# Kernel tuning notes

Measured on AMD Instinct MI355X. Metric: run time of the kernel, lower is better.

The kernel has to match this reference:

```python
import jax, jax.numpy as jnp
import numpy as np

B, L, P = 16, 128, 8192
ALPHA = 2.0            # current_alpha (softness_start)
STEP_PROGRESS = 0.5    # > 0.15 so e_ghost == 0; t_gate = sigmoid(3.0)
PROT_RADII = np.array([1.7, 1.55, 1.52, 1.8], dtype=np.float32)
PROT_EPS = np.array([0.1, 0.1, 0.15, 0.2], dtype=np.float32)
VDW_RADII = np.array([1.7, 1.55, 1.52, 1.8, 1.1, 1.47, 1.75, 1.85, 1.98], dtype=np.float32)
EPSILON = np.array([0.086, 0.17, 0.21, 0.25, 0.015, 0.061, 0.265, 0.32, 0.4], dtype=np.float32)


def setup_inputs() -> dict:
    key = jax.random.key(0)
    ks = jax.random.split(key, 6)
    # positions spread over ~ a binding-pocket-sized box so distances are realistic
    pos_L = jax.random.normal(ks[0], (B, L, 3), jnp.float32) * 8.0
    pos_P = jax.random.normal(ks[1], (B, P, 3), jnp.float32) * 8.0
    q_L = jax.random.normal(ks[2], (B, L), jnp.float32) * 0.3
    q_P = jax.random.normal(ks[3], (B, P), jnp.float32) * 0.3
    x_L = jax.random.uniform(ks[4], (B, L, 9), jnp.float32)
    x_L = x_L / jnp.sum(x_L, axis=-1, keepdims=True)  # type probabilities
    x_P = jax.random.uniform(ks[5], (B, P, 4), jnp.float32)
    x_P = x_P / jnp.sum(x_P, axis=-1, keepdims=True)
    return {
        'pos_L': pos_L, 'pos_P': pos_P, 'q_L': q_L, 'q_P': q_P,
        'x_L': x_L, 'x_P': x_P,
        'vdw_radii': jnp.asarray(VDW_RADII), 'epsilon_tbl': jnp.asarray(EPSILON),
    }


def reference(pos_L, pos_P, q_L, q_P, x_L, x_P, vdw_radii, epsilon_tbl):
    sg = jax.lax.stop_gradient
    # pairwise geometry: diff [B,L,P,3]
    diff = pos_L[:, :, None, :] - pos_P[:, None, :, :]
    dist_sq = jnp.sum(diff * diff, axis=-1)              # [B,L,P]
    dist = jnp.sqrt(dist_sq + 1e-8)
    # mixed vdw radii
    type_probs_L = x_L[..., :9]
    radii_L = type_probs_L @ vdw_radii                    # [B,L]
    radii_P = x_P[..., :4] @ jnp.asarray(PROT_RADII)      # [B,P]
    sigma_ij = radii_L[:, :, None] + radii_P[:, None, :]  # [B,L,P]
    # soft-core distance
    soft_dist = jnp.sqrt(dist_sq + ALPHA * sigma_ij * sigma_ij + 1e-8)
    # electrostatics (dielectric = 4.0), tanh-clamped
    e_elec_raw = 332.06 * q_L[:, :, None] * q_P[:, None, :] / (4.0 * soft_dist)
    e_elec = 200.0 * jnp.tanh(e_elec_raw / 200.0)
    # LJ 12-6 with geometric-mean epsilon
    eps_L = jax.nn.relu(type_probs_L @ epsilon_tbl)       # [B,L]
    eps_P = x_P[..., :4] @ jnp.asarray(PROT_EPS)          # [B,P]
    eps_ij = jnp.sqrt(eps_L[:, :, None] * eps_P[:, None, :] + 1e-8)
    ratio = jnp.minimum(sigma_ij / (soft_dist + 1e-8), 5.0)
    ratio6 = ratio ** 6
    ratio12 = ratio6 * ratio6
    e_vdw_raw = 4.0 * eps_ij * (ratio12 - ratio6)
    e_pos = 500.0 * jnp.tanh(jax.nn.relu(e_vdw_raw) / 500.0)
    e_neg = -10.0 * jnp.tanh(jax.nn.relu(-e_vdw_raw) / 10.0)
    e_vdw_grad = e_pos + e_neg
    # smooth 12 A cutoff
    dist_mask = jax.nn.sigmoid((12.0 - dist) * 2.0)
    e_soft = jnp.sum((e_elec + e_vdw_grad) * dist_mask, axis=(1, 2))  # [B]
    # hydrophobic surface attraction (carbon-carbon)
    mask_cc = type_probs_L[..., 0][:, :, None] * x_P[..., 0][:, None, :]
    hsa_term = 1.0 / (1.0 + (dist / 4.0) ** 4)
    e_hsa = jnp.sum(-0.5 * mask_cc * hsa_term * dist_mask, axis=(1, 2))
    # Pauli repulsion, gated by step progress
    t_gate = jax.nn.sigmoid(jnp.float32((STEP_PROGRESS - 0.2) * 10.0))
    overlap = jax.nn.relu(sigma_ij * 0.6 - dist)
    e_pauli = t_gate * 100.0 * jnp.sum(overlap * overlap, axis=(1, 2))
    # e_ghost = 0 since STEP_PROGRESS >= 0.15
    e_ghost = jnp.zeros_like(e_pauli)
    e_raw = e_soft + 5.0 * e_hsa + e_pauli + e_ghost
    e_raw = jnp.nan_to_num(e_raw, nan=0.0)
    # logging quantities (detached in the original)
    log_vdw = jnp.clip(sg(e_vdw_raw), -10.0, 500.0)
    log_soft_core = jnp.sum((sg(e_elec) + log_vdw) * sg(dist_mask), axis=(1, 2))
    e_soft_log = jnp.clip(log_soft_core + 5.0 * sg(e_hsa), -500.0, 5000.0)
    e_hard_log = jnp.minimum(sg(e_pauli + e_ghost), 10000.0)
    log_energy_val = jnp.minimum(e_soft_log + e_hard_log, 1000000.0)
    return e_raw, e_hard_log, jnp.float32(ALPHA), log_energy_val
```

## Files before the change

kernel.cpp:

```cpp
#include <hip/hip_runtime.h>
#include <math.h>

#define NB 16
#define NL 128
#define NP 8192
#define CHUNKS 32
#define THREADS 256
#define LSPLIT 2
#define LHALF (NL / LSPLIT)

__device__ __forceinline__ float fexp2(float x) { return __builtin_amdgcn_exp2f(x); }
__device__ __forceinline__ float frcp(float x)  { return __builtin_amdgcn_rcpf(x); }
__device__ __forceinline__ float frsq(float x)  { return __builtin_amdgcn_rsqf(x); }
__device__ __forceinline__ float fsqrt_(float x){ return __builtin_amdgcn_sqrtf(x); }

__global__ __launch_bounds__(THREADS) void physics_main(
    const float* __restrict__ pos_L, const float* __restrict__ pos_P,
    const float* __restrict__ q_L,   const float* __restrict__ q_P,
    const float* __restrict__ x_L,   const float* __restrict__ x_P,
    const float* __restrict__ vdw_radii, const float* __restrict__ eps_tbl,
    float* __restrict__ partial)
{
    const int b     = blockIdx.y;
    const int chunk = blockIdx.x;
    const int z     = blockIdx.z;
    const int tid   = threadIdx.x;

    __shared__ float4 lig[LHALF][2];
    __shared__ float red[4][3];

    if (tid < LHALF) {
        const int base = b * NL + z * LHALF + tid;
        float px = pos_L[base * 3 + 0];
        float py = pos_L[base * 3 + 1];
        float pz = pos_L[base * 3 + 2];
        float aq = 83.015f * q_L[base];
        float rad = 0.0f, ep = 0.0f;
        #pragma unroll
        for (int j = 0; j < 9; ++j) {
            float v = x_L[base * 9 + j];
            rad = fmaf(v, vdw_radii[j], rad);
            ep  = fmaf(v, eps_tbl[j],  ep);
        }
        float seL4 = 4.0f * fsqrt_(fmaxf(ep, 0.0f));
        float x0   = x_L[base * 9 + 0];
        lig[tid][0] = make_float4(px, py, pz, aq);
        lig[tid][1] = make_float4(rad, seL4, x0, 0.0f);
    }
    __syncthreads();

    const int p  = chunk * THREADS + tid;
    const int pb = b * NP + p;
    const float ppx = pos_P[pb * 3 + 0];
    const float ppy = pos_P[pb * 3 + 1];
    const float ppz = pos_P[pb * 3 + 2];
    const float qP  = q_P[pb];
    const float4 xp = ((const float4*)x_P)[pb];
    const float rP  = 1.7f * xp.x + 1.55f * xp.y + 1.52f * xp.z + 1.8f * xp.w;
    const float epP = 0.1f * xp.x + 0.10f * xp.y + 0.15f * xp.z + 0.2f * xp.w;
    const float seP = fsqrt_(epP);
    const float xP0 = xp.x;

    float s1 = 0.0f, s2 = 0.0f, s3 = 0.0f;

    #pragma unroll 4
    for (int l = 0; l < LHALF; ++l) {
        const float4 a  = lig[l][0];
        const float4 bv = lig[l][1];

        float dx = a.x - ppx, dy = a.y - ppy, dz = a.z - ppz;
        float ds = fmaf(dx, dx, fmaf(dy, dy, fmaf(dz, dz, 1e-8f)));
        float dist = fsqrt_(ds);

        float sigma = bv.x + rP;
        float sd2 = fmaf(sigma, sigma + sigma, ds);
        float inv_sd = frsq(sd2);

        float v  = (a.w * qP) * inv_sd;
        float u  = 0.005f * v;
        float u2 = u * u;
        float pf = fmaf(u2, fmaf(u2, 0.13333333f, -0.33333333f), 1.0f);
        float e_elec = v * pf;

        float ratio = sigma * inv_sd;
        float r2 = ratio * ratio;
        float r6 = r2 * r2 * r2;
        float ev = (bv.y * seP) * r6 * (r6 - 1.0f);
        float addend = e_elec + ev;

        float m  = fminf(fmaf(dist, 2.8853901f, -34.624681f), 30.0f);
        float A  = 1.0f + fexp2(m);
        float tq = ds * 0.0625f;
        float Bh = fmaf(tq, tq, 1.0f);
        float r  = frcp(A * Bh);
        float dm = Bh * r;

        s1 = fmaf(addend, dm, s1);
        s2 = fmaf(bv.z, r, s2);

        float ov = fmaxf(fmaf(sigma, 0.6f, -dist), 0.0f);
        s3 = fmaf(ov, ov, s3);
    }
    s2 *= xP0;

    #pragma unroll
    for (int off = 32; off > 0; off >>= 1) {
        s1 += __shfl_down(s1, off);
        s2 += __shfl_down(s2, off);
        s3 += __shfl_down(s3, off);
    }
    const int lane = tid & 63;
    const int wid  = tid >> 6;
    if (lane == 0) {
        red[wid][0] = s1; red[wid][1] = s2; red[wid][2] = s3;
    }
    __syncthreads();
    if (tid == 0) {
        float r0 = red[0][0] + red[1][0] + red[2][0] + red[3][0];
        float r1 = red[0][1] + red[1][1] + red[2][1] + red[3][1];
        float r2_ = red[0][2] + red[1][2] + red[2][2] + red[3][2];
        float* dst = partial + ((size_t)((b * CHUNKS + chunk) * LSPLIT + z)) * 4;
        dst[0] = r0; dst[1] = r1; dst[2] = r2_;
    }
}

__global__ void physics_final(const float* __restrict__ partial, float* __restrict__ out)
{
    const int b = threadIdx.x;
    if (b == 0) out[2 * NB] = 2.0f;
    if (b >= NB) return;
    float s1 = 0.0f, s2 = 0.0f, s3 = 0.0f;
    for (int c = 0; c < CHUNKS * LSPLIT; ++c) {
        const float* src = partial + ((size_t)(b * CHUNKS * LSPLIT + c)) * 4;
        s1 += src[0]; s2 += src[1]; s3 += src[2];
    }
    const float TG100 = 95.25741268224334f;
    float e_pauli = TG100 * s3;
    float e_hsa5  = -2.5f * s2;
    float e_raw = s1 + e_hsa5 + e_pauli;
    if (e_raw != e_raw) e_raw = 0.0f;
    float e_hard_log = fminf(e_pauli, 10000.0f);
    float e_soft_log = fminf(fmaxf(s1 + e_hsa5, -500.0f), 5000.0f);
    float log_energy = fminf(e_soft_log + e_hard_log, 1000000.0f);

    out[b]              = e_raw;
    out[NB + b]         = e_hard_log;
    out[2 * NB + 1 + b] = log_energy;
}

extern "C" void kernel_launch(void* const* d_in, const int* in_sizes, int n_in,
                              void* d_out, int out_size, void* d_ws, size_t ws_size,
                              hipStream_t stream)
{
    const float* pos_L = (const float*)d_in[0];
    const float* pos_P = (const float*)d_in[1];
    const float* q_L   = (const float*)d_in[2];
    const float* q_P   = (const float*)d_in[3];
    const float* x_L   = (const float*)d_in[4];
    const float* x_P   = (const float*)d_in[5];
    const float* vdw   = (const float*)d_in[6];
    const float* epst  = (const float*)d_in[7];
    float* out = (float*)d_out;
    float* partial = (float*)d_ws;

    dim3 grid(CHUNKS, NB, LSPLIT);
    physics_main<<<grid, THREADS, 0, stream>>>(pos_L, pos_P, q_L, q_P, x_L, x_P,
                                               vdw, epst, partial);
    physics_final<<<1, 64, 0, stream>>>(partial, out);
}
```

Before: 94.39 us.

## Vectorize ligand loop with packed float2 math and split ligands four ways

Rewrites the inner pair loop so each thread processes two ligand atoms at once using 2-wide vector FMA types, which can map to packed FP32 instructions on CDNA. The shared-memory ligand table is relaid out in SoA-pair form to feed these vectors. The ligand dimension is split into four grid slices instead of two for more blocks. The min clamp on the exp argument is removed, and the tanh polynomial is folded into new constants. Transcendentals stay scalar, so only the arithmetic portion gains packing.

```diff
diff --git a/kernel.cpp b/kernel.cpp
--- a/kernel.cpp
+++ b/kernel.cpp
@@ -6,13 +6,17 @@
 #define NP 8192
 #define CHUNKS 32
 #define THREADS 256
-#define LSPLIT 2
+#define LSPLIT 4
 #define LHALF (NL / LSPLIT)
+#define LPAIR (LHALF / 2)
+
+typedef float v2 __attribute__((ext_vector_type(2)));
 
 __device__ __forceinline__ float fexp2(float x) { return __builtin_amdgcn_exp2f(x); }
 __device__ __forceinline__ float frcp(float x)  { return __builtin_amdgcn_rcpf(x); }
 __device__ __forceinline__ float frsq(float x)  { return __builtin_amdgcn_rsqf(x); }
 __device__ __forceinline__ float fsqrt_(float x){ return __builtin_amdgcn_sqrtf(x); }
+__device__ __forceinline__ v2 vfma(v2 a, v2 b, v2 c) { return __builtin_elementwise_fma(a, b, c); }
 
 __global__ __launch_bounds__(THREADS) void physics_main(
     const float* __restrict__ pos_L, const float* __restrict__ pos_P,
@@ -26,7 +30,8 @@
     const int z     = blockIdx.z;
     const int tid   = threadIdx.x;
 
-    __shared__ float4 lig[LHALF][2];
+    __shared__ float4 lig[LPAIR][3];
+    __shared__ float2 lig3[LPAIR];
     __shared__ float red[4][3];
 
     if (tid < LHALF) {
@@ -42,10 +47,17 @@
             rad = fmaf(v, vdw_radii[j], rad);
             ep  = fmaf(v, eps_tbl[j],  ep);
         }
-        float seL4 = 4.0f * fsqrt_(fmaxf(ep, 0.0f));
-        float x0   = x_L[base * 9 + 0];
-        lig[tid][0] = make_float4(px, py, pz, aq);
-        lig[tid][1] = make_float4(rad, seL4, x0, 0.0f);
+        float se4 = 4.0f * fsqrt_(fmaxf(ep, 0.0f));
+        float x0  = x_L[base * 9 + 0];
+        const int i = tid >> 1, s = tid & 1;
+        float* L = (float*)lig;
+        L[i * 12 + 0 + s] = px;
+        L[i * 12 + 2 + s] = py;
+        L[i * 12 + 4 + s] = pz;
+        L[i * 12 + 6 + s] = aq;
+        L[i * 12 + 8 + s] = rad;
+        L[i * 12 + 10 + s] = se4;
+        ((float*)lig3)[i * 2 + s] = x0;
     }
     __syncthreads();
 
@@ -61,47 +73,64 @@
     const float seP = fsqrt_(epP);
     const float xP0 = xp.x;
 
-    float s1 = 0.0f, s2 = 0.0f, s3 = 0.0f;
+    v2 s1v = (v2)0.0f, s2v = (v2)0.0f, s3v = (v2)0.0f;
+    const v2 onev = (v2)1.0f;
+    const v2 C1 = (v2)(-8.3333333e-6f);
+    const v2 C2 = (v2)(8.3333333e-11f);
 
     #pragma unroll 4
-    for (int l = 0; l < LHALF; ++l) {
-        const float4 a  = lig[l][0];
-        const float4 bv = lig[l][1];
-
-        float dx = a.x - ppx, dy = a.y - ppy, dz = a.z - ppz;
-        float ds = fmaf(dx, dx, fmaf(dy, dy, fmaf(dz, dz, 1e-8f)));
-        float dist = fsqrt_(ds);
-
-        float sigma = bv.x + rP;
-        float sd2 = fmaf(sigma, sigma + sigma, ds);
-        float inv_sd = frsq(sd2);
-
-        float v  = (a.w * qP) * inv_sd;
-        float u  = 0.005f * v;
-        float u2 = u * u;
-        float pf = fmaf(u2, fmaf(u2, 0.13333333f, -0.33333333f), 1.0f);
-        float e_elec = v * pf;
-
-        float ratio = sigma * inv_sd;
-        float r2 = ratio * ratio;
-        float r6 = r2 * r2 * r2;
-        float ev = (bv.y * seP) * r6 * (r6 - 1.0f);
-        float addend = e_elec + ev;
-
-        float m  = fminf(fmaf(dist, 2.8853901f, -34.624681f), 30.0f);
-        float A  = 1.0f + fexp2(m);
-        float tq = ds * 0.0625f;
-        float Bh = fmaf(tq, tq, 1.0f);
-        float r  = frcp(A * Bh);
-        float dm = Bh * r;
-
-        s1 = fmaf(addend, dm, s1);
-        s2 = fmaf(bv.z, r, s2);
-
-        float ov = fmaxf(fmaf(sigma, 0.6f, -dist), 0.0f);
-        s3 = fmaf(ov, ov, s3);
-    }
-    s2 *= xP0;
+    for (int i = 0; i < LPAIR; ++i) {
+        const float4 t0 = lig[i][0];
+        const float4 t1 = lig[i][1];
+        const float4 t2 = lig[i][2];
+        const float2 t3 = lig3[i];
+
+        v2 lx; lx.x = t0.x; lx.y = t0.y;
+        v2 ly; ly.x = t0.z; ly.y = t0.w;
+        v2 lz; lz.x = t1.x; lz.y = t1.y;
+        v2 laq; laq.x = t1.z; laq.y = t1.w;
+        v2 lrad; lrad.x = t2.x; lrad.y = t2.y;
+        v2 lse; lse.x = t2.z; lse.y = t2.w;
+        v2 lx0; lx0.x = t3.x; lx0.y = t3.y;
+
+        v2 dx = lx - ppx, dy = ly - ppy, dz = lz - ppz;
+        v2 ds = vfma(dx, dx, vfma(dy, dy, vfma(dz, dz, (v2)1e-8f)));
+        v2 dist; dist.x = fsqrt_(ds.x); dist.y = fsqrt_(ds.y);
+
+        v2 sigma = lrad + rP;
+        v2 sigsq = sigma * sigma;
+        v2 sd2 = vfma(sigsq, (v2)2.0f, ds);
+        v2 inv; inv.x = frsq(sd2.x); inv.y = frsq(sd2.y);
+
+        v2 v = laq * (qP * inv);
+        v2 w = v * v;
+        v2 pf = vfma(w, vfma(w, C2, C1), onev);
+        v2 e_elec = v * pf;
+
+        v2 r2 = sigsq * (inv * inv);
+        v2 r6 = r2 * r2 * r2;
+        v2 t126 = vfma(r6, r6, -r6);
+        v2 ev = (lse * seP) * t126;
+        v2 addend = e_elec + ev;
+
+        v2 m = vfma(dist, (v2)2.8853901f, (v2)(-34.624681f));
+        v2 A; A.x = fexp2(m.x); A.y = fexp2(m.y);
+        A = A + onev;
+        v2 tq = ds * 0.0625f;
+        v2 Bh = vfma(tq, tq, onev);
+        v2 AB = A * Bh;
+        v2 r; r.x = frcp(AB.x); r.y = frcp(AB.y);
+        v2 dm = Bh * r;
+
+        s1v = vfma(addend, dm, s1v);
+        s2v = vfma(lx0, r, s2v);
+        v2 ov = __builtin_elementwise_max(vfma(sigma, (v2)0.6f, -dist), (v2)0.0f);
+        s3v = vfma(ov, ov, s3v);
+    }
+
+    float s1 = s1v.x + s1v.y;
+    float s2 = (s2v.x + s2v.y) * xP0;
+    float s3 = s3v.x + s3v.y;
 
     #pragma unroll
     for (int off = 32; off > 0; off >>= 1) {
@@ -130,6 +159,7 @@
     if (b == 0) out[2 * NB] = 2.0f;
     if (b >= NB) return;
     float s1 = 0.0f, s2 = 0.0f, s3 = 0.0f;
+    #pragma unroll 8
     for (int c = 0; c < CHUNKS * LSPLIT; ++c) {
         const float* src = partial + ((size_t)(b * CHUNKS * LSPLIT + c)) * 4;
         s1 += src[0]; s2 += src[1]; s3 += src[2];
```

After: 92.04 us. 1.03x faster.
